# Optimization experiments

Hardware: AMD Instinct MI355X
Metric: run time of the kernel (lower is better)

Reference implementation:

```python
import jax, jax.numpy as jnp
import numpy as np

B, T, D, DIM = 32, 2048, 1024, 1024


def setup_inputs() -> dict:
    key = jax.random.key(0)
    ks = jax.random.split(key, 7)
    def glorot(k, shape):
        lim = np.sqrt(6.0 / (shape[0] + shape[1]))
        return jax.random.uniform(k, shape, jnp.float32, -lim, lim)
    return {
        "input_states": jax.random.normal(ks[0], (B, T, D), jnp.float32),
        "last_state": jax.random.normal(ks[1], (B, D), jnp.float32),
        "Wy": glorot(ks[2], (D, DIM)),
        "Wh": glorot(ks[3], (D, DIM)),
        "w": glorot(ks[4], (DIM, 1)),
        "Wp": glorot(ks[5], (D, DIM)),
        "Wx": glorot(ks[6], (D, DIM)),
    }


def reference(input_states, last_state, Wy, Wh, w, Wp, Wx):
    # hs: (B,T,dim); last_state projection broadcast over T (the original
    # tiles last_state via a ones-matmul; a plain broadcast is the same math)
    hs = jnp.einsum("btd,de->bte", input_states, Wy)
    hproj = last_state @ Wh                      # (B,dim)
    m = jax.nn.relu(hs + hproj[:, None, :])      # (B,T,dim)
    scores = jnp.einsum("bte,eo->bt", m, w[:, :1])  # squeeze last dim
    alpha = jax.nn.softmax(scores, axis=-1)      # (B,T)
    r = jnp.einsum("bt,btd->bd", alpha, input_states)
    out = jax.nn.relu(r @ Wp + last_state @ Wx)  # (B,dim)
    return out
```

## Files before the change

### kernel.cpp

```cpp
#include <hip/hip_runtime.h>
#include <hip/hip_bf16.h>
#include <stdint.h>

#define BB 32
#define TT 2048
#define DD 1024
#define DIMQ 1024
#define MTOT (BB*TT)

typedef __attribute__((ext_vector_type(8))) __bf16 bf16x8;
typedef __attribute__((ext_vector_type(4))) float f32x4;

__device__ __forceinline__ unsigned short f2bf(float f) {
    unsigned int u = __float_as_uint(f);
    u += 0x7FFF + ((u >> 16) & 1);
    return (unsigned short)(u >> 16);
}
__device__ __forceinline__ float bf2f(unsigned short s) {
    return __uint_as_float(((unsigned int)s) << 16);
}

__device__ __forceinline__ void load_lds16(const void* g, void* l) {
    __builtin_amdgcn_global_load_lds(
        (const __attribute__((address_space(1))) unsigned int*)g,
        (__attribute__((address_space(3))) unsigned int*)l,
        16, 0, 0);
}

__global__ void cast_x(const float* __restrict__ x, unsigned short* __restrict__ xb) {
    long i = ((long)blockIdx.x * blockDim.x + threadIdx.x) * 4;
    float4 a = *(const float4*)(x + i);
    ushort4 o;
    o.x = f2bf(a.x); o.y = f2bf(a.y); o.z = f2bf(a.z); o.w = f2bf(a.w);
    *(ushort4*)(xb + i) = o;
}

__global__ void transpose_cast(const float* __restrict__ Wsrc, unsigned short* __restrict__ Wdst) {
    __shared__ float tile[32][33];
    int bx = blockIdx.x * 32;
    int by = blockIdx.y * 32;
    int tx = threadIdx.x & 31;
    int ty4 = (threadIdx.x >> 5) * 4;
    #pragma unroll
    for (int r = 0; r < 4; r++)
        tile[ty4 + r][tx] = Wsrc[(size_t)(by + ty4 + r) * DIMQ + bx + tx];
    __syncthreads();
    #pragma unroll
    for (int r = 0; r < 4; r++)
        Wdst[(size_t)(bx + ty4 + r) * DD + by + tx] = f2bf(tile[tx][ty4 + r]);
}

__global__ void vecmat2(const float* __restrict__ last,
                        const float* __restrict__ Wh, const float* __restrict__ Wx,
                        float* __restrict__ hproj, float* __restrict__ lsWx) {
    __shared__ float vs[DD];
    __shared__ float red[4][64];
    int b = blockIdx.y;
    int e0 = blockIdx.x * 64;
    const float* Mat = blockIdx.z ? Wx : Wh;
    float* outp = blockIdx.z ? lsWx : hproj;
    int tid = threadIdx.x;
    for (int d = tid; d < DD; d += 256) vs[d] = last[b * DD + d];
    __syncthreads();
    int e = tid & 63, dg = tid >> 6;
    int d0 = dg * 256;
    const float* Mp = Mat + (size_t)d0 * DIMQ + e0 + e;
    float acc = 0.f;
    #pragma unroll 8
    for (int d = 0; d < 256; d++) acc += vs[d0 + d] * Mp[(size_t)d * DIMQ];
    red[dg][e] = acc;
    __syncthreads();
    if (dg == 0)
        outp[b * DIMQ + e0 + e] = red[0][e] + red[1][e] + red[2][e] + red[3][e];
}

__global__ __launch_bounds__(256, 2)
void gemm_scores(const unsigned short* __restrict__ Xb,
                 const unsigned short* __restrict__ WyT,
                 const float* __restrict__ hproj,
                 const float* __restrict__ wvec,
                 float* __restrict__ partials) {
    __shared__ unsigned short Alds[4096];
    __shared__ unsigned short Blds[8192];
    __shared__ float lp[128];

    int x = blockIdx.x;
    int mtile = x >> 2, ntile = x & 3;
    int tid = threadIdx.x;
    int lane = tid & 63;
    int wave = tid >> 6;

    if (tid < 128) lp[tid] = 0.f;

    const int rowA0 = mtile * 128;
    const int colB0 = ntile * 256;

    int rsel = lane & 15;
    int koff = (lane >> 4) * 8;
    int s0 = tid >> 6;

    const unsigned short* Ag0 = Xb  + (size_t)(rowA0 + s0 * 16 + rsel) * DD + koff;
    const unsigned short* Ag1 = Ag0 + (size_t)64 * DD;
    const unsigned short* Bg0 = WyT + (size_t)(colB0 + s0 * 16 + rsel) * DD + koff;
    const unsigned short* Bg1 = Bg0 + (size_t)64 * DD;
    const unsigned short* Bg2 = Bg0 + (size_t)128 * DD;
    const unsigned short* Bg3 = Bg0 + (size_t)192 * DD;

    unsigned short* Al0 = &Alds[tid * 8];
    unsigned short* Al1 = &Alds[(tid + 256) * 8];
    unsigned short* Bl0 = &Blds[tid * 8];
    unsigned short* Bl1 = &Blds[(tid + 256) * 8];
    unsigned short* Bl2 = &Blds[(tid + 512) * 8];
    unsigned short* Bl3 = &Blds[(tid + 768) * 8];

    int wr = wave >> 1;
    int wc = wave & 1;

    f32x4 acc[4][8] = {};

    for (int kk = 0; kk < DD; kk += 32) {
        load_lds16(Ag0 + kk, Al0);
        load_lds16(Ag1 + kk, Al1);
        load_lds16(Bg0 + kk, Bl0);
        load_lds16(Bg1 + kk, Bl1);
        load_lds16(Bg2 + kk, Bl2);
        load_lds16(Bg3 + kk, Bl3);
        __syncthreads();

        bf16x8 af[4], bfr[8];
        #pragma unroll
        for (int i = 0; i < 4; i++)
            af[i] = *reinterpret_cast<const bf16x8*>(&Alds[((wr * 4 + i) * 64 + lane) * 8]);
        #pragma unroll
        for (int j = 0; j < 8; j++)
            bfr[j] = *reinterpret_cast<const bf16x8*>(&Blds[((wc * 8 + j) * 64 + lane) * 8]);
        #pragma unroll
        for (int i = 0; i < 4; i++)
            #pragma unroll
            for (int j = 0; j < 8; j++)
                acc[i][j] = __builtin_amdgcn_mfma_f32_16x16x32_bf16(af[i], bfr[j], acc[i][j], 0, 0, 0);
        __syncthreads();
    }

    int b = rowA0 / TT;
    int q = lane >> 4, l15 = lane & 15;

    float hpv[8], wvv[8];
    #pragma unroll
    for (int j = 0; j < 8; j++) {
        int n = colB0 + wc * 128 + j * 16 + l15;
        hpv[j] = hproj[b * DIMQ + n];
        wvv[j] = wvec[n];
    }

    #pragma unroll
    for (int i = 0; i < 4; i++) {
        f32x4 s = {0.f, 0.f, 0.f, 0.f};
        #pragma unroll
        for (int j = 0; j < 8; j++) {
            #pragma unroll
            for (int r = 0; r < 4; r++) {
                float v = acc[i][j][r] + hpv[j];
                v = v > 0.f ? v : 0.f;
                s[r] += v * wvv[j];
            }
        }
        #pragma unroll
        for (int off = 1; off < 16; off <<= 1) {
            s[0] += __shfl_xor(s[0], off);
            s[1] += __shfl_xor(s[1], off);
            s[2] += __shfl_xor(s[2], off);
            s[3] += __shfl_xor(s[3], off);
        }
        if (l15 == 0) {
            int mrow = wr * 64 + i * 16 + q * 4;
            atomicAdd(&lp[mrow + 0], s[0]);
            atomicAdd(&lp[mrow + 1], s[1]);
            atomicAdd(&lp[mrow + 2], s[2]);
            atomicAdd(&lp[mrow + 3], s[3]);
        }
    }
    __syncthreads();
    if (tid < 128)
        partials[(size_t)ntile * MTOT + rowA0 + tid] = lp[tid];
}

__global__ void softmax_alpha(const float* __restrict__ partials, float* __restrict__ alpha) {
    __shared__ float wred[4];
    __shared__ float wsum[4];
    int b = blockIdx.x;
    int tid = threadIdx.x;
    float s[8];
    float mx = -1e30f;
    #pragma unroll
    for (int c = 0; c < 8; c++) {
        int t = b * TT + tid + c * 256;
        float v = 0.f;
        #pragma unroll
        for (int p = 0; p < 4; p++) v += partials[(size_t)p * MTOT + t];
        s[c] = v;
        mx = fmaxf(mx, v);
    }
    for (int off = 32; off; off >>= 1) mx = fmaxf(mx, __shfl_xor(mx, off));
    if ((tid & 63) == 0) wred[tid >> 6] = mx;
    __syncthreads();
    mx = fmaxf(fmaxf(wred[0], wred[1]), fmaxf(wred[2], wred[3]));
    float sum = 0.f;
    #pragma unroll
    for (int c = 0; c < 8; c++) { s[c] = expf(s[c] - mx); sum += s[c]; }
    for (int off = 32; off; off >>= 1) sum += __shfl_xor(sum, off);
    if ((tid & 63) == 0) wsum[tid >> 6] = sum;
    __syncthreads();
    sum = wsum[0] + wsum[1] + wsum[2] + wsum[3];
    float inv = 1.f / sum;
    #pragma unroll
    for (int c = 0; c < 8; c++) alpha[b * TT + tid + c * 256] = s[c] * inv;
}

__global__ void weighted_sum(const unsigned short* __restrict__ Xb,
                             const float* __restrict__ alpha,
                             float* __restrict__ r_part) {
    __shared__ float al[128];
    int tc = blockIdx.x, b = blockIdx.y, tid = threadIdx.x;
    if (tid < 128) al[tid] = alpha[b * TT + tc * 128 + tid];
    __syncthreads();
    int d0 = tid * 4;
    const unsigned short* base = Xb + ((size_t)(b * TT + tc * 128)) * DD + d0;
    f32x4 acc = {0.f, 0.f, 0.f, 0.f};
    #pragma unroll 2
    for (int t = 0; t < 128; t++) {
        ushort4 xv = *(const ushort4*)(base + (size_t)t * DD);
        float a_ = al[t];
        acc[0] += a_ * bf2f(xv.x);
        acc[1] += a_ * bf2f(xv.y);
        acc[2] += a_ * bf2f(xv.z);
        acc[3] += a_ * bf2f(xv.w);
    }
    float* o = r_part + ((size_t)tc * BB + b) * DD + d0;
    *(float4*)o = *(float4*)&acc;
}

__global__ void final_out(const float* __restrict__ r_part, const float* __restrict__ Wp,
                          const float* __restrict__ lsWx, float* __restrict__ out) {
    __shared__ float rs[DD];
    __shared__ float red[4][64];
    int b = blockIdx.y;
    int e0 = blockIdx.x * 64;
    int tid = threadIdx.x;
    for (int d = tid; d < DD; d += 256) {
        float v = 0.f;
        #pragma unroll
        for (int p = 0; p < 16; p++) v += r_part[((size_t)p * BB + b) * DD + d];
        rs[d] = v;
    }
    __syncthreads();
    int e = tid & 63, dg = tid >> 6;
    int d0 = dg * 256;
    const float* Mp = Wp + (size_t)d0 * DIMQ + e0 + e;
    float acc = 0.f;
    #pragma unroll 8
    for (int d = 0; d < 256; d++) acc += rs[d0 + d] * Mp[(size_t)d * DIMQ];
    red[dg][e] = acc;
    __syncthreads();
    if (dg == 0) {
        float v = red[0][e] + red[1][e] + red[2][e] + red[3][e]
                + lsWx[b * DIMQ + e0 + e];
        out[b * DIMQ + e0 + e] = fmaxf(v, 0.f);
    }
}

extern "C" void kernel_launch(void* const* d_in, const int* in_sizes, int n_in,
                              void* d_out, int out_size, void* d_ws, size_t ws_size,
                              hipStream_t stream) {
    const float* x    = (const float*)d_in[0];
    const float* last = (const float*)d_in[1];
    const float* Wy   = (const float*)d_in[2];
    const float* Wh   = (const float*)d_in[3];
    const float* w    = (const float*)d_in[4];
    const float* Wp   = (const float*)d_in[5];
    const float* Wx   = (const float*)d_in[6];
    float* out = (float*)d_out;

    char* ws = (char*)d_ws;
    unsigned short* Xb   = (unsigned short*)(ws);
    unsigned short* WyT  = (unsigned short*)(ws + 134217728);
    float* hproj         = (float*)(ws + 136314880);
    float* lsWx          = (float*)(ws + 136445952);
    float* partials      = (float*)(ws + 136577024);
    float* alpha         = (float*)(ws + 137625600);
    float* r_part        = (float*)(ws + 137887744);

    cast_x<<<BB*TT*DD/4/256, 256, 0, stream>>>(x, Xb);
    transpose_cast<<<dim3(32, 32), 256, 0, stream>>>(Wy, WyT);
    vecmat2<<<dim3(DIMQ/64, BB, 2), 256, 0, stream>>>(last, Wh, Wx, hproj, lsWx);
    gemm_scores<<<512 * 4, 256, 0, stream>>>(Xb, WyT, hproj, w, partials);
    softmax_alpha<<<BB, 256, 0, stream>>>(partials, alpha);
    weighted_sum<<<dim3(TT/128, BB), 256, 0, stream>>>(Xb, alpha, r_part);
    final_out<<<dim3(DIMQ/64, BB), 256, 0, stream>>>(r_part, Wp, lsWx, out);
}
```

Before: 642.9 us.

## Rewrite scores GEMM as 256x256 tile, 8-wave double-buffered pipelined kernel

Replaces the 128x256-tile, 4-wave single-buffered GEMM with a 256x256-tile, 512-thread kernel. It double-buffers LDS, interleaves global-to-LDS staging with MFMA quadrants under explicit barriers and waitcnts, and raises wave priority around the MFMA blocks. Block indices are remapped so neighbouring tiles land on the same XCD for L2 reuse. The goal is to hide load latency and cut redundant global traffic in the dominant GEMM. The cost is 128KB of LDS, higher register pressure, and fragile hand-written wait counts.

New measurement: 626.1 us. -2.6%, faster.

```diff
diff --git a/kernel.cpp b/kernel.cpp
--- a/kernel.cpp
+++ b/kernel.cpp
@@ -74,95 +74,123 @@
         outp[b * DIMQ + e0 + e] = red[0][e] + red[1][e] + red[2][e] + red[3][e];
 }
 
-__global__ __launch_bounds__(256, 2)
+__global__ __launch_bounds__(512, 2)
 void gemm_scores(const unsigned short* __restrict__ Xb,
                  const unsigned short* __restrict__ WyT,
                  const float* __restrict__ hproj,
                  const float* __restrict__ wvec,
                  float* __restrict__ partials) {
-    __shared__ unsigned short Alds[4096];
-    __shared__ unsigned short Blds[8192];
-    __shared__ float lp[128];
-
-    int x = blockIdx.x;
-    int mtile = x >> 2, ntile = x & 3;
+    __shared__ unsigned short lds[65536];
+    __shared__ float lp[256];
+
     int tid = threadIdx.x;
     int lane = tid & 63;
     int wave = tid >> 6;
-
-    if (tid < 128) lp[tid] = 0.f;
-
-    const int rowA0 = mtile * 128;
-    const int colB0 = ntile * 256;
-
-    int rsel = lane & 15;
-    int koff = (lane >> 4) * 8;
-    int s0 = tid >> 6;
-
-    const unsigned short* Ag0 = Xb  + (size_t)(rowA0 + s0 * 16 + rsel) * DD + koff;
-    const unsigned short* Ag1 = Ag0 + (size_t)64 * DD;
-    const unsigned short* Bg0 = WyT + (size_t)(colB0 + s0 * 16 + rsel) * DD + koff;
-    const unsigned short* Bg1 = Bg0 + (size_t)64 * DD;
-    const unsigned short* Bg2 = Bg0 + (size_t)128 * DD;
-    const unsigned short* Bg3 = Bg0 + (size_t)192 * DD;
-
-    unsigned short* Al0 = &Alds[tid * 8];
-    unsigned short* Al1 = &Alds[(tid + 256) * 8];
-    unsigned short* Bl0 = &Blds[tid * 8];
-    unsigned short* Bl1 = &Blds[(tid + 256) * 8];
-    unsigned short* Bl2 = &Blds[(tid + 512) * 8];
-    unsigned short* Bl3 = &Blds[(tid + 768) * 8];
-
-    int wr = wave >> 1;
-    int wc = wave & 1;
-
-    f32x4 acc[4][8] = {};
-
-    for (int kk = 0; kk < DD; kk += 32) {
-        load_lds16(Ag0 + kk, Al0);
-        load_lds16(Ag1 + kk, Al1);
-        load_lds16(Bg0 + kk, Bl0);
-        load_lds16(Bg1 + kk, Bl1);
-        load_lds16(Bg2 + kk, Bl2);
-        load_lds16(Bg3 + kk, Bl3);
-        __syncthreads();
-
-        bf16x8 af[4], bfr[8];
-        #pragma unroll
-        for (int i = 0; i < 4; i++)
-            af[i] = *reinterpret_cast<const bf16x8*>(&Alds[((wr * 4 + i) * 64 + lane) * 8]);
-        #pragma unroll
-        for (int j = 0; j < 8; j++)
-            bfr[j] = *reinterpret_cast<const bf16x8*>(&Blds[((wc * 8 + j) * 64 + lane) * 8]);
-        #pragma unroll
-        for (int i = 0; i < 4; i++)
-            #pragma unroll
-            for (int j = 0; j < 8; j++)
-                acc[i][j] = __builtin_amdgcn_mfma_f32_16x16x32_bf16(af[i], bfr[j], acc[i][j], 0, 0, 0);
-        __syncthreads();
-    }
-
-    int b = rowA0 / TT;
+    int wr = wave >> 2;
+    int wc = wave & 3;
+
+    int bidx = blockIdx.x;
+    int rr = bidx & 255, rnd = bidx >> 8;
+    int xcd = rr & 7, slot = rr >> 3;
+    int ntile = slot & 3;
+    int mtile = rnd * 64 + xcd * 8 + (slot >> 2);
+
+    if (tid < 256) lp[tid] = 0.f;
+
+    int ssub = wave >> 1, sks = wave & 1;
+    const unsigned short* aG = Xb  + (size_t)(mtile * 256 + ssub * 16 + (lane & 15)) * DD + sks * 32 + (lane >> 4) * 8;
+    const unsigned short* bG = WyT + (size_t)(ntile * 256 + ssub * 16 + (lane & 15)) * DD + sks * 32 + (lane >> 4) * 8;
+    unsigned short* ldsAst = &lds[(ssub * 128 + sks * 64 + lane) * 8];
+    unsigned short* ldsBst = ldsAst + 16384;
+
+    const unsigned short* aRd = &lds[wr * 8192 + lane * 8];
+    const unsigned short* bRd = &lds[16384 + (wc >> 1) * 8192 + (wc & 1) * 4096 + lane * 8];
+
+#define STAGE_A(B_, H_, T_) { \
+    const unsigned short* g_ = aG + (size_t)(H_) * 131072 + (T_) * 64; \
+    load_lds16(g_,         ldsAst + (B_) * 32768 + (H_) * 8192);       \
+    load_lds16(g_ + 65536, ldsAst + (B_) * 32768 + (H_) * 8192 + 4096); }
+#define STAGE_B(B_, H_, T_) { \
+    const unsigned short* g_ = bG + (size_t)(H_) * 131072 + (T_) * 64; \
+    load_lds16(g_,         ldsBst + (B_) * 32768 + (H_) * 8192);       \
+    load_lds16(g_ + 65536, ldsBst + (B_) * 32768 + (H_) * 8192 + 4096); }
+
+    f32x4 acc[8][4] = {};
+    bf16x8 af[4][2], bfr[4][2];
+
+#define LDA(B_, MH) { \
+    _Pragma("unroll") for (int i_ = 0; i_ < 4; i_++) \
+    _Pragma("unroll") for (int k_ = 0; k_ < 2; k_++) \
+        af[i_][k_] = *reinterpret_cast<const bf16x8*>(aRd + (B_) * 32768 + ((MH) * 4 + i_) * 1024 + k_ * 512); }
+#define LDB(B_, NH) { \
+    _Pragma("unroll") for (int j_ = 0; j_ < 2; j_++) \
+    _Pragma("unroll") for (int k_ = 0; k_ < 2; k_++) \
+        bfr[(NH) * 2 + j_][k_] = *reinterpret_cast<const bf16x8*>(bRd + (B_) * 32768 + ((NH) * 2 + j_) * 1024 + k_ * 512); }
+#define MFMA_Q(MH, NH) { \
+    _Pragma("unroll") for (int k_ = 0; k_ < 2; k_++) \
+    _Pragma("unroll") for (int i_ = 0; i_ < 4; i_++) \
+    _Pragma("unroll") for (int j_ = 0; j_ < 2; j_++) \
+        acc[(MH) * 4 + i_][(NH) * 2 + j_] = __builtin_amdgcn_mfma_f32_16x16x32_bf16( \
+            af[i_][k_], bfr[(NH) * 2 + j_][k_], acc[(MH) * 4 + i_][(NH) * 2 + j_], 0, 0, 0); }
+
+#define BAR() __builtin_amdgcn_s_barrier()
+#define LGKM0() { asm volatile("s_waitcnt lgkmcnt(0)" ::: "memory"); __builtin_amdgcn_sched_barrier(0); }
+#define VM4() asm volatile("s_waitcnt vmcnt(4)" ::: "memory")
+#define PRIO1() __builtin_amdgcn_s_setprio(1)
+#define PRIO0() __builtin_amdgcn_s_setprio(0)
+
+    STAGE_B(0, 0, 0); STAGE_B(0, 1, 0);
+    STAGE_A(0, 0, 0); STAGE_A(0, 1, 0);
+    STAGE_B(1, 0, 1); STAGE_B(1, 1, 1);
+    VM4();
+    BAR();
+
+    for (int it = 0; it < 8; ++it) {
+        int t1  = 2 * it + 1;
+        int tp0 = 2 * it + 2; if (tp0 > 14) tp0 = 14;
+        int tp1 = 2 * it + 3; if (tp1 > 15) tp1 = 15;
+
+        LDA(0, 0); LDB(0, 0); STAGE_A(1, 0, t1);
+        BAR(); LGKM0(); PRIO1(); MFMA_Q(0, 0); PRIO0(); BAR();
+        LDB(0, 1); STAGE_A(1, 1, t1);
+        BAR(); LGKM0(); PRIO1(); MFMA_Q(0, 1); PRIO0(); BAR();
+        LDA(0, 1); STAGE_B(0, 0, tp0);
+        BAR(); LGKM0(); PRIO1(); MFMA_Q(1, 1); PRIO0(); BAR();
+        STAGE_B(0, 1, tp0);
+        BAR(); PRIO1(); MFMA_Q(1, 0); PRIO0(); VM4(); BAR();
+        LDA(1, 0); LDB(1, 0); STAGE_A(0, 0, tp0);
+        BAR(); LGKM0(); PRIO1(); MFMA_Q(0, 0); PRIO0(); BAR();
+        LDB(1, 1); STAGE_A(0, 1, tp0);
+        BAR(); LGKM0(); PRIO1(); MFMA_Q(0, 1); PRIO0(); BAR();
+        LDA(1, 1); STAGE_B(1, 0, tp1);
+        BAR(); LGKM0(); PRIO1(); MFMA_Q(1, 1); PRIO0(); BAR();
+        STAGE_B(1, 1, tp1);
+        BAR(); PRIO1(); MFMA_Q(1, 0); PRIO0(); VM4(); BAR();
+    }
+
+    __syncthreads();
+
+    int bIdx = mtile >> 3;
     int q = lane >> 4, l15 = lane & 15;
 
-    float hpv[8], wvv[8];
-    #pragma unroll
-    for (int j = 0; j < 8; j++) {
-        int n = colB0 + wc * 128 + j * 16 + l15;
-        hpv[j] = hproj[b * DIMQ + n];
-        wvv[j] = wvec[n];
-    }
-
-    #pragma unroll
-    for (int i = 0; i < 4; i++) {
+    float hpv[4], wvv[4];
+    #pragma unroll
+    for (int nf = 0; nf < 4; nf++) {
+        int n = ntile * 256 + wc * 64 + nf * 16 + l15;
+        hpv[nf] = hproj[bIdx * DIMQ + n];
+        wvv[nf] = wvec[n];
+    }
+
+    #pragma unroll
+    for (int m = 0; m < 8; m++) {
         f32x4 s = {0.f, 0.f, 0.f, 0.f};
         #pragma unroll
-        for (int j = 0; j < 8; j++) {
+        for (int nf = 0; nf < 4; nf++) {
             #pragma unroll
             for (int r = 0; r < 4; r++) {
-                float v = acc[i][j][r] + hpv[j];
+                float v = acc[m][nf][r] + hpv[nf];
                 v = v > 0.f ? v : 0.f;
-                s[r] += v * wvv[j];
+                s[r] += v * wvv[nf];
             }
         }
         #pragma unroll
@@ -173,7 +201,7 @@
             s[3] += __shfl_xor(s[3], off);
         }
         if (l15 == 0) {
-            int mrow = wr * 64 + i * 16 + q * 4;
+            int mrow = wr * 128 + m * 16 + q * 4;
             atomicAdd(&lp[mrow + 0], s[0]);
             atomicAdd(&lp[mrow + 1], s[1]);
             atomicAdd(&lp[mrow + 2], s[2]);
@@ -181,8 +209,19 @@
         }
     }
     __syncthreads();
-    if (tid < 128)
-        partials[(size_t)ntile * MTOT + rowA0 + tid] = lp[tid];
+    if (tid < 256)
+        partials[(size_t)ntile * MTOT + mtile * 256 + tid] = lp[tid];
+
+#undef STAGE_A
+#undef STAGE_B
+#undef LDA
+#undef LDB
+#undef MFMA_Q
+#undef BAR
+#undef LGKM0
+#undef VM4
+#undef PRIO1
+#undef PRIO0
 }
 
 __global__ void softmax_alpha(const float* __restrict__ partials, float* __restrict__ alpha) {
@@ -293,7 +332,7 @@
     cast_x<<<BB*TT*DD/4/256, 256, 0, stream>>>(x, Xb);
     transpose_cast<<<dim3(32, 32), 256, 0, stream>>>(Wy, WyT);
     vecmat2<<<dim3(DIMQ/64, BB, 2), 256, 0, stream>>>(last, Wh, Wx, hproj, lsWx);
-    gemm_scores<<<512 * 4, 256, 0, stream>>>(Xb, WyT, hproj, w, partials);
+    gemm_scores<<<1024, 512, 0, stream>>>(Xb, WyT, hproj, w, partials);
     softmax_alpha<<<BB, 256, 0, stream>>>(partials, alpha);
     weighted_sum<<<dim3(TT/128, BB), 256, 0, stream>>>(Xb, alpha, r_part);
     final_out<<<dim3(DIMQ/64, BB), 256, 0, stream>>>(r_part, Wp, lsWx, out);
```
